# Performance work log

Measured on AMD Instinct MI355X. Metric: run time of the kernel, lower is better.

Reference implementation:

```python
import jax, jax.numpy as jnp
import numpy as np

B, C, H, W = 32, 256, 64, 64
MH = 8
E = 524288
TEMPERATURE = 0.1
LN_EPS = 1e-5


def setup_inputs() -> dict:
    key = jax.random.key(0)
    ks = jax.random.split(key, 6)
    n_nodes = B * H * W
    scale = 1.0 / np.sqrt(C).astype(np.float32)
    img = jax.random.normal(ks[0], (B, C, H, W), jnp.float32)
    all_edge = jax.random.randint(ks[1], (2, E), 0, n_nodes, dtype=jnp.int64)
    Wp = jax.random.normal(ks[2], (C, C), jnp.float32) * scale
    bp = jnp.zeros((C,), jnp.float32)
    Wg = jax.random.normal(ks[3], (C, C), jnp.float32) * scale
    bg = jnp.zeros((C,), jnp.float32)
    ln_gamma = jnp.ones((C,), jnp.float32)
    ln_beta = jnp.zeros((C,), jnp.float32)
    diff_query = jax.random.normal(ks[4], (1, 1, C), jnp.float32) * scale  # xavier-ish
    return {"img": img, "all_edge": all_edge, "Wp": Wp, "bp": bp,
            "Wg": Wg, "bg": bg, "ln_gamma": ln_gamma, "ln_beta": ln_beta,
            "diff_query": diff_query, "mask_head": MH}


def _gcn_conv(x, row, col, Wg, bg, num_nodes):
    # PyG GCNConv with add_self_loops=True, symmetric normalization.
    loop = jnp.arange(num_nodes, dtype=row.dtype)
    row = jnp.concatenate([row, loop])
    col = jnp.concatenate([col, loop])
    deg = jnp.zeros((num_nodes,), x.dtype).at[col].add(1.0)
    dinv = jnp.where(deg > 0, jax.lax.rsqrt(deg), 0.0)
    norm = dinv[row] * dinv[col]                      # [E+N]
    xl = x @ Wg                                       # [N, C]
    msg = xl[row] * norm[:, None]                     # gather + scale
    agg = jax.ops.segment_sum(msg, col, num_segments=num_nodes)
    return agg + bg


def reference(img, all_edge, Wp, bp, Wg, bg, ln_gamma, ln_beta, diff_query, mask_head):
    b, c, h, w = img.shape
    node_num = h * w
    num_nodes = b * node_num
    hd = c // mask_head
    # [B,C,H,W] -> [B, N, C]
    x = jnp.transpose(img, (0, 2, 3, 1)).reshape(b, node_num, c)
    x = x @ Wp + bp
    x = x.reshape(num_nodes, c)
    g = _gcn_conv(x, all_edge[0], all_edge[1], Wg, bg, num_nodes)
    g = jax.nn.gelu(g, approximate=False)             # nn.GELU (exact)
    g = g + x
    mu = jnp.mean(g, axis=-1, keepdims=True)
    var = jnp.mean(jnp.square(g - mu), axis=-1, keepdims=True)
    img_graph = (g - mu) * jax.lax.rsqrt(var + LN_EPS) * ln_gamma + ln_beta
    # multi-head adjacency: query [B*MH, 1, hd], keys [B*MH, N, hd]
    q = jnp.broadcast_to(diff_query, (b, 1, c)).reshape(b * mask_head, 1, hd)
    k = img_graph.reshape(b, node_num, mask_head, hd)
    k = jnp.transpose(k, (0, 2, 1, 3)).reshape(b * mask_head, node_num, hd)
    adj = jnp.einsum('bod,bnd->bon', q, k) / TEMPERATURE
    adj = jax.nn.softmax(adj, axis=-1)
    return img_graph, adj
```

## Files before the change

kernel.cpp:

```cpp
#include <hip/hip_runtime.h>

typedef unsigned short u16;
typedef __attribute__((ext_vector_type(8))) short short8;
typedef __attribute__((ext_vector_type(4))) float f32x4;
typedef __attribute__((ext_vector_type(16))) float f32x16;

#define AS1C(p) ((const __attribute__((address_space(1))) void*)(p))
#define AS3(p)  ((__attribute__((address_space(3))) void*)(p))

constexpr int CC    = 256;
constexpr int HWSZ  = 4096;
constexpr int NNODE = 131072;
constexpr int EEDG  = 524288;
constexpr int CAP   = 32;

__device__ __forceinline__ float bf2f(u16 h){ unsigned u = ((unsigned)h)<<16; float f; __builtin_memcpy(&f,&u,4); return f; }
__device__ __forceinline__ u16 f2bf(float f){ unsigned u; __builtin_memcpy(&u,&f,4); return (u16)((u + 0x7FFFu + ((u>>16)&1u))>>16); }
__device__ __forceinline__ float gelu_exact(float v){ return 0.5f*v*(1.0f + erff(v*0.7071067811865476f)); }

__device__ __forceinline__ void unpack8(uint4 q, float f[8]){
  unsigned w0=q.x,w1=q.y,w2=q.z,w3=q.w;
  unsigned l0=w0<<16, h0=w0&0xffff0000u, l1=w1<<16, h1=w1&0xffff0000u;
  unsigned l2=w2<<16, h2=w2&0xffff0000u, l3=w3<<16, h3=w3&0xffff0000u;
  __builtin_memcpy(&f[0],&l0,4); __builtin_memcpy(&f[1],&h0,4);
  __builtin_memcpy(&f[2],&l1,4); __builtin_memcpy(&f[3],&h1,4);
  __builtin_memcpy(&f[4],&l2,4); __builtin_memcpy(&f[5],&h2,4);
  __builtin_memcpy(&f[6],&l3,4); __builtin_memcpy(&f[7],&h3,4);
}

__global__ __launch_bounds__(256) void transpose_split(const float* __restrict__ src,
                                                       u16* __restrict__ dhi, u16* __restrict__ dlo,
                                                       int R, int Ccols, size_t sb_in, size_t sb_out)
{
  __shared__ float t[64][65];
  const float* s = src + blockIdx.z*sb_in + (size_t)(blockIdx.y*64)*Ccols + blockIdx.x*64;
  size_t obase   = blockIdx.z*sb_out + (size_t)(blockIdx.x*64)*R + blockIdx.y*64;
  int tid = threadIdx.x;
  for (int i=0;i<4;++i){
    int idx = i*256 + tid;
    int r = idx>>4, q = idx&15;
    float4 v = *(const float4*)(s + (size_t)r*Ccols + q*4);
    t[r][q*4+0]=v.x; t[r][q*4+1]=v.y; t[r][q*4+2]=v.z; t[r][q*4+3]=v.w;
  }
  __syncthreads();
  for (int i=0;i<2;++i){
    int idx = i*256 + tid;
    int rr = idx>>3, ch = idx&7;
    u16 hi[8], lo[8];
    for (int j=0;j<8;++j){
      float f = t[ch*8+j][rr];
      u16 h = f2bf(f); hi[j] = h;
      lo[j] = f2bf(f - bf2f(h));
    }
    *(uint4*)(dhi + obase + (size_t)rr*R + ch*8) = *(uint4*)hi;
    if (dlo) *(uint4*)(dlo + obase + (size_t)rr*R + ch*8) = *(uint4*)lo;
  }
}

__global__ __launch_bounds__(256,2) void gemm_img(const float* __restrict__ img,
                                                  const u16* __restrict__ Bt,
                                                  const float* __restrict__ bias,
                                                  u16* __restrict__ C)
{
  __shared__ float Afp[2][32*128];
  __shared__ u16   Bs[2][128*32];
  const int tid = threadIdx.x, wid = tid>>6, lane = tid&63;
  const int row0 = blockIdx.x*128, col0 = blockIdx.y*128;
  const int bb = row0 >> 12, hw0 = row0 & 4095;
  const float* abase = img + (size_t)bb*CC*HWSZ + hw0;
  const int wm = wid>>1, wn = wid&1;
  const int l31 = lane&31, lh = lane>>5;

  f32x16 acc[2][2];
  #pragma unroll
  for (int i=0;i<2;++i)
    #pragma unroll
    for (int j=0;j<2;++j)
      #pragma unroll
      for (int e=0;e<16;++e) acc[i][j][e]=0.f;

#define STAGE_IMG(buf, kt)                                                             \
  {                                                                                    \
    _Pragma("unroll")                                                                  \
    for (int it=0; it<4; ++it){                                                        \
      int qb = (it*4+wid)*64;                                                          \
      int q  = qb + lane;                                                              \
      int c  = q>>5, qq = q&31;                                                        \
      __builtin_amdgcn_global_load_lds(AS1C(abase + (size_t)((kt)+c)*HWSZ + qq*4),     \
                                       AS3(&Afp[buf][qb*4]), 16, 0, 0);                \
    }                                                                                  \
    _Pragma("unroll")                                                                  \
    for (int it=0; it<2; ++it){                                                        \
      int qb = (it*4+wid)*64;                                                          \
      int q  = qb + lane;                                                              \
      int m  = q>>2, sc = q&3;                                                         \
      int gs = sc ^ ((m>>1)&3);                                                        \
      __builtin_amdgcn_global_load_lds(AS1C(Bt + (size_t)(col0+m)*256 + (kt) + gs*8),  \
                                       AS3(&Bs[buf][qb*8]), 16, 0, 0);                 \
    }                                                                                  \
  }

  STAGE_IMG(0, 0)
  asm volatile("s_waitcnt vmcnt(0)" ::: "memory");
  __syncthreads();

  for (int t=0; t<8; ++t) {
    int cur = t&1;
    if (t<7) STAGE_IMG(cur^1, (t+1)*32)

    short8 ah[2][2], al[2][2], bfr[2][2];
    #pragma unroll
    for (int fm=0; fm<2; ++fm)
      #pragma unroll
      for (int kh=0; kh<2; ++kh) {
        int r  = wm*64 + fm*32 + l31;
        int cb = kh*16 + lh*8;
        #pragma unroll
        for (int j=0; j<8; ++j) {
          float f = Afp[cur][(cb+j)*128 + r];
          unsigned u; __builtin_memcpy(&u,&f,4);
          ah[fm][kh][j] = (short)(u>>16);
          unsigned uh = u & 0xffff0000u;
          float fh; __builtin_memcpy(&fh,&uh,4);
          float fl = f - fh;
          unsigned ul; __builtin_memcpy(&ul,&fl,4);
          al[fm][kh][j] = (short)(ul>>16);
        }
      }
    #pragma unroll
    for (int fn=0; fn<2; ++fn)
      #pragma unroll
      for (int kh=0; kh<2; ++kh) {
        int col = wn*64 + fn*32 + l31;
        int sb  = (kh*2 + lh) ^ ((col>>1)&3);
        bfr[fn][kh] = *(const short8*)&Bs[cur][col*32 + sb*8];
      }
    #pragma unroll
    for (int kh=0; kh<2; ++kh)
      #pragma unroll
      for (int fm=0; fm<2; ++fm)
        #pragma unroll
        for (int fn=0; fn<2; ++fn) {
          acc[fm][fn] = __builtin_amdgcn_mfma_f32_32x32x16_bf16(ah[fm][kh], bfr[fn][kh], acc[fm][fn], 0, 0, 0);
          acc[fm][fn] = __builtin_amdgcn_mfma_f32_32x32x16_bf16(al[fm][kh], bfr[fn][kh], acc[fm][fn], 0, 0, 0);
        }
    asm volatile("s_waitcnt vmcnt(0)" ::: "memory");
    __syncthreads();
  }
#undef STAGE_IMG

  #pragma unroll
  for (int fn=0; fn<2; ++fn) {
    int col = col0 + wn*64 + fn*32 + l31;
    float bv = bias ? bias[col] : 0.f;
    #pragma unroll
    for (int fm=0; fm<2; ++fm) {
      int rbase = row0 + wm*64 + fm*32 + 4*lh;
      #pragma unroll
      for (int reg=0; reg<16; ++reg) {
        int row = rbase + (reg&3) + 8*(reg>>2);
        C[(size_t)row*256 + col] = f2bf(acc[fm][fn][reg] + bv);
      }
    }
  }
}

__global__ __launch_bounds__(256,2) void gemm1p(const u16* __restrict__ A,
                                                const u16* __restrict__ Bt,
                                                u16* __restrict__ C)
{
  __shared__ u16 As[2][128*32];
  __shared__ u16 Bs[2][128*32];
  const int tid = threadIdx.x, wid = tid>>6, lane = tid&63;
  const int row0 = blockIdx.x*128, col0 = blockIdx.y*128;
  const int wm = wid>>1, wn = wid&1;
  const int l31 = lane&31, lh = lane>>5;

  f32x16 acc[2][2];
  #pragma unroll
  for (int i=0;i<2;++i)
    #pragma unroll
    for (int j=0;j<2;++j)
      #pragma unroll
      for (int e=0;e<16;++e) acc[i][j][e]=0.f;

#define STAGE_AB(buf, kt)                                                              \
  {                                                                                    \
    _Pragma("unroll")                                                                  \
    for (int it=0; it<2; ++it){                                                        \
      int qb = (it*4+wid)*64;                                                          \
      int q  = qb + lane;                                                              \
      int m  = q>>2, sc = q&3;                                                         \
      int gs = sc ^ ((m>>1)&3);                                                        \
      __builtin_amdgcn_global_load_lds(AS1C(A  + (size_t)(row0+m)*256 + (kt) + gs*8),  \
                                       AS3(&As[buf][qb*8]), 16, 0, 0);                 \
      __builtin_amdgcn_global_load_lds(AS1C(Bt + (size_t)(col0+m)*256 + (kt) + gs*8),  \
                                       AS3(&Bs[buf][qb*8]), 16, 0, 0);                 \
    }                                                                                  \
  }

  STAGE_AB(0, 0)
  asm volatile("s_waitcnt vmcnt(0)" ::: "memory");
  __syncthreads();

  for (int t=0; t<8; ++t) {
    int cur = t&1;
    if (t<7) STAGE_AB(cur^1, (t+1)*32)

    short8 af[2][2], bfr[2][2];
    #pragma unroll
    for (int fm=0; fm<2; ++fm)
      #pragma unroll
      for (int kh=0; kh<2; ++kh) {
        int row = wm*64 + fm*32 + l31;
        int sa  = (kh*2 + lh) ^ ((row>>1)&3);
        af[fm][kh] = *(const short8*)&As[cur][row*32 + sa*8];
      }
    #pragma unroll
    for (int fn=0; fn<2; ++fn)
      #pragma unroll
      for (int kh=0; kh<2; ++kh) {
        int col = wn*64 + fn*32 + l31;
        int sb  = (kh*2 + lh) ^ ((col>>1)&3);
        bfr[fn][kh] = *(const short8*)&Bs[cur][col*32 + sb*8];
      }
    #pragma unroll
    for (int kh=0; kh<2; ++kh)
      #pragma unroll
      for (int fm=0; fm<2; ++fm)
        #pragma unroll
        for (int fn=0; fn<2; ++fn)
          acc[fm][fn] = __builtin_amdgcn_mfma_f32_32x32x16_bf16(af[fm][kh], bfr[fn][kh], acc[fm][fn], 0, 0, 0);
    asm volatile("s_waitcnt vmcnt(0)" ::: "memory");
    __syncthreads();
  }
#undef STAGE_AB

  #pragma unroll
  for (int fn=0; fn<2; ++fn) {
    int col = col0 + wn*64 + fn*32 + l31;
    #pragma unroll
    for (int fm=0; fm<2; ++fm) {
      int rbase = row0 + wm*64 + fm*32 + 4*lh;
      #pragma unroll
      for (int reg=0; reg<16; ++reg) {
        int row = rbase + (reg&3) + 8*(reg>>2);
        C[(size_t)row*256 + col] = f2bf(acc[fm][fn][reg]);
      }
    }
  }
}

__global__ void fill_all(const int* __restrict__ row, const int* __restrict__ col,
                         int* __restrict__ cur, int* __restrict__ bucket){
  int e = blockIdx.x*256 + threadIdx.x;
  if (e >= EEDG) return;
  int c = col[e];
  int s = atomicAdd(&cur[c], 1);
  if (s < CAP) bucket[(size_t)c*CAP + s] = row[e];
}
__global__ void calc_dinv(const int* __restrict__ cnt, float* __restrict__ dinv){
  int n = blockIdx.x*256 + threadIdx.x;
  if (n < NNODE) dinv[n] = rsqrtf((float)cnt[n] + 1.0f);
}

__global__ __launch_bounds__(256) void fused_agg(
    const u16* __restrict__ xl, const u16* __restrict__ xhi,
    const int* __restrict__ cnt, const float* __restrict__ dinv, const int* __restrict__ bucket,
    const float* __restrict__ bgv, const float* __restrict__ gam, const float* __restrict__ bet,
    const float* __restrict__ qv, float* __restrict__ outg, float* __restrict__ logits)
{
  const int wid = threadIdx.x>>6, lane = threadIdx.x&63;
  const int half = lane>>5, sl = lane&31;
  const int n = blockIdx.x*8 + wid*2 + half;
  const int c0 = sl*8;
  const float dn = dinv[n];
  int lim = cnt[n]; if (lim > CAP) lim = CAP;

  int rl = bucket[(size_t)n*CAP + sl];
  if (sl >= lim) rl = n;
  float wl = (sl < lim) ? dinv[rl]*dn : 0.0f;

  float xv[8];
  uint4 qh = *(const uint4*)(xhi + (size_t)n*256 + c0);

  float a[8];
  {
    uint4 q = *(const uint4*)(xl + (size_t)n*256 + c0);
    unpack8(q, a);
    float wself = dn*dn;
    #pragma unroll
    for (int j=0;j<8;++j) a[j] *= wself;
  }

  int limR = (lim + 3) & ~3;
  for (int s=0; s<limR; s+=4) {
    int b0 = half*32 + s;
    int  r0 = __shfl(rl, b0),   r1 = __shfl(rl, b0+1);
    int  r2 = __shfl(rl, b0+2), r3 = __shfl(rl, b0+3);
    float w0 = __shfl(wl, b0),   w1 = __shfl(wl, b0+1);
    float w2 = __shfl(wl, b0+2), w3 = __shfl(wl, b0+3);
    uint4 q0 = *(const uint4*)(xl + (size_t)r0*256 + c0);
    uint4 q1 = *(const uint4*)(xl + (size_t)r1*256 + c0);
    uint4 q2 = *(const uint4*)(xl + (size_t)r2*256 + c0);
    uint4 q3 = *(const uint4*)(xl + (size_t)r3*256 + c0);
    float f0[8], f1[8], f2[8], f3[8];
    unpack8(q0, f0); unpack8(q1, f1); unpack8(q2, f2); unpack8(q3, f3);
    #pragma unroll
    for (int j=0;j<8;++j) a[j] += f0[j]*w0 + f1[j]*w1 + f2[j]*w2 + f3[j]*w3;
  }

  unpack8(qh, xv);

  float4 b0v = *(const float4*)(bgv + c0), b1v = *(const float4*)(bgv + c0 + 4);
  float bgs[8] = {b0v.x,b0v.y,b0v.z,b0v.w,b1v.x,b1v.y,b1v.z,b1v.w};
  float g[8];
  float s1 = 0.f, s2 = 0.f;
  #pragma unroll
  for (int j=0;j<8;++j){
    g[j] = gelu_exact(a[j] + bgs[j]) + xv[j];
    s1 += g[j]; s2 += g[j]*g[j];
  }
  #pragma unroll
  for (int off=16; off; off>>=1){ s1 += __shfl_xor(s1, off); s2 += __shfl_xor(s2, off); }
  float mu  = s1*(1.0f/256.0f);
  float var = s2*(1.0f/256.0f) - mu*mu;
  float inv = rsqrtf(var + 1e-5f);

  float4 g0 = *(const float4*)(gam + c0), g1 = *(const float4*)(gam + c0 + 4);
  float4 e0 = *(const float4*)(bet + c0), e1 = *(const float4*)(bet + c0 + 4);
  float gms[8] = {g0.x,g0.y,g0.z,g0.w,g1.x,g1.y,g1.z,g1.w};
  float bts[8] = {e0.x,e0.y,e0.z,e0.w,e1.x,e1.y,e1.z,e1.w};
  float y[8];
  #pragma unroll
  for (int j=0;j<8;++j) y[j] = (g[j]-mu)*inv*gms[j] + bts[j];

  f32x4 o0 = {y[0],y[1],y[2],y[3]}, o1 = {y[4],y[5],y[6],y[7]};
  __builtin_nontemporal_store(o0, (f32x4*)(outg + (size_t)n*256 + c0));
  __builtin_nontemporal_store(o1, (f32x4*)(outg + (size_t)n*256 + c0 + 4));

  float4 q0 = *(const float4*)(qv + c0), q1 = *(const float4*)(qv + c0 + 4);
  float qs[8] = {q0.x,q0.y,q0.z,q0.w,q1.x,q1.y,q1.z,q1.w};
  float dq = 0.f;
  #pragma unroll
  for (int j=0;j<8;++j) dq += y[j]*qs[j];
  dq += __shfl_xor(dq,1); dq += __shfl_xor(dq,2);
  if ((sl&3)==0){
    int b = n>>12, p = n&4095, h = sl>>2;
    logits[(size_t)(b*8+h)*4096 + p] = dq*10.0f;
  }
}

__global__ __launch_bounds__(256) void softmax_rows(const float* __restrict__ logits, float* __restrict__ outa){
  int r = blockIdx.x;
  const float* p = logits + (size_t)r*4096;
  int tid = threadIdx.x;
  int wid = tid>>6, lane = tid&63;
  __shared__ float redm[4];
  __shared__ float reds[4];
  float v[16];
  float mx = -1e30f;
  for (int i=0;i<16;++i){ v[i] = p[tid + i*256]; mx = fmaxf(mx, v[i]); }
  for (int off=32; off; off>>=1) mx = fmaxf(mx, __shfl_xor(mx, off));
  if (lane==0) redm[wid]=mx;
  __syncthreads();
  mx = fmaxf(fmaxf(redm[0],redm[1]), fmaxf(redm[2],redm[3]));
  float sum = 0.f;
  for (int i=0;i<16;++i){ v[i] = expf(v[i]-mx); sum += v[i]; }
  for (int off=32; off; off>>=1) sum += __shfl_xor(sum, off);
  if (lane==0) reds[wid]=sum;
  __syncthreads();
  sum = reds[0]+reds[1]+reds[2]+reds[3];
  float rinv = 1.0f/sum;
  for (int i=0;i<16;++i) outa[(size_t)r*4096 + tid + i*256] = v[i]*rinv;
}

extern "C" void kernel_launch(void* const* d_in, const int* in_sizes, int n_in,
                              void* d_out, int out_size, void* d_ws, size_t ws_size,
                              hipStream_t stream)
{
  const float* img  = (const float*)d_in[0];
  const int* edges  = (const int*)d_in[1];
  const float* Wp   = (const float*)d_in[2];
  const float* bp   = (const float*)d_in[3];
  const float* Wg   = (const float*)d_in[4];
  const float* bg   = (const float*)d_in[5];
  const float* lng  = (const float*)d_in[6];
  const float* lnb  = (const float*)d_in[7];
  const float* dq   = (const float*)d_in[8];
  char* ws = (char*)d_ws;

  constexpr size_t REG  = (size_t)NNODE*CC*2;
  constexpr size_t WTS  = 2u*131072;
  constexpr size_t GBLK = 524288u*2 + (size_t)NNODE*CAP*4 + (size_t)256*4096*4;
  if (ws_size < 2*REG + WTS + GBLK) return;

  u16* x_hi = (u16*)(ws + 0);
  u16* xl   = (u16*)(ws + REG);
  char* wts  = ws + 2*REG;
  char* gblk = wts + WTS;

  u16* WpT_hi = (u16*)(wts);
  u16* WgT_hi = (u16*)(wts + 131072);
  int*   cur    = (int*)(gblk);
  float* dinv   = (float*)(gblk + 524288);
  int*   bucket = (int*)(gblk + 1048576);
  float* logits = (float*)(gblk + 1048576 + (size_t)NNODE*CAP*4);

  transpose_split<<<dim3(4,4,1), 256, 0, stream>>>(Wp, WpT_hi, nullptr, 256, 256, 0, 0);
  transpose_split<<<dim3(4,4,1), 256, 0, stream>>>(Wg, WgT_hi, nullptr, 256, 256, 0, 0);

  hipMemsetAsync(cur, 0, 524288, stream);
  fill_all <<<2048, 256, 0, stream>>>(edges, edges+EEDG, cur, bucket);
  calc_dinv<<<512,  256, 0, stream>>>(cur, dinv);

  gemm_img<<<dim3(1024,2), 256, 0, stream>>>(img, WpT_hi, bp, x_hi);
  gemm1p<<<dim3(1024,2), 256, 0, stream>>>(x_hi, WgT_hi, xl);

  float* outg = (float*)d_out;
  float* outa = (float*)d_out + (size_t)NNODE*CC;
  fused_agg<<<NNODE/8, 256, 0, stream>>>(xl, x_hi, cur, dinv, bucket,
                                         bg, lng, lnb, dq, outg, logits);
  softmax_rows<<<256, 256, 0, stream>>>(logits, outa);
}
```

Measured before the change: 242.5 us.

## Retile GEMMs to 64x256 blocks covering full output width

Both projection GEMMs switch from 128x128 tiles on a 2D grid to 64-row by 256-column tiles on a 1D grid. Each block now reads its A rows (the image, or the projected features) once instead of twice, and each of the four waves owns a 64-column slice. This cuts duplicate A-side global traffic, especially the fp32 image reads with hi/lo splitting, at the cost of staging more B per block and larger LDS for B. The aggregation kernel also swaps its nontemporal output stores for plain float4 stores.

```diff
diff --git a/kernel.cpp b/kernel.cpp
--- a/kernel.cpp
+++ b/kernel.cpp
@@ -62,13 +62,12 @@
                                                   const float* __restrict__ bias,
                                                   u16* __restrict__ C)
 {
-  __shared__ float Afp[2][32*128];
-  __shared__ u16   Bs[2][128*32];
+  __shared__ float Afp[2][32*64];
+  __shared__ u16   Bs[2][256*32];
   const int tid = threadIdx.x, wid = tid>>6, lane = tid&63;
-  const int row0 = blockIdx.x*128, col0 = blockIdx.y*128;
+  const int row0 = blockIdx.x*64;
   const int bb = row0 >> 12, hw0 = row0 & 4095;
   const float* abase = img + (size_t)bb*CC*HWSZ + hw0;
-  const int wm = wid>>1, wn = wid&1;
   const int l31 = lane&31, lh = lane>>5;
 
   f32x16 acc[2][2];
@@ -81,21 +80,21 @@
 
 #define STAGE_IMG(buf, kt)                                                             \
   {                                                                                    \
+    _Pragma("unroll")                                                                  \
+    for (int it=0; it<2; ++it){                                                        \
+      int qb = (it*4+wid)*64;                                                          \
+      int q  = qb + lane;                                                              \
+      int c  = q>>4, mq = q&15;                                                        \
+      __builtin_amdgcn_global_load_lds(AS1C(abase + (size_t)((kt)+c)*HWSZ + mq*4),     \
+                                       AS3(&Afp[buf][qb*4]), 16, 0, 0);                \
+    }                                                                                  \
     _Pragma("unroll")                                                                  \
     for (int it=0; it<4; ++it){                                                        \
       int qb = (it*4+wid)*64;                                                          \
       int q  = qb + lane;                                                              \
-      int c  = q>>5, qq = q&31;                                                        \
-      __builtin_amdgcn_global_load_lds(AS1C(abase + (size_t)((kt)+c)*HWSZ + qq*4),     \
-                                       AS3(&Afp[buf][qb*4]), 16, 0, 0);                \
-    }                                                                                  \
-    _Pragma("unroll")                                                                  \
-    for (int it=0; it<2; ++it){                                                        \
-      int qb = (it*4+wid)*64;                                                          \
-      int q  = qb + lane;                                                              \
       int m  = q>>2, sc = q&3;                                                         \
       int gs = sc ^ ((m>>1)&3);                                                        \
-      __builtin_amdgcn_global_load_lds(AS1C(Bt + (size_t)(col0+m)*256 + (kt) + gs*8),  \
+      __builtin_amdgcn_global_load_lds(AS1C(Bt + (size_t)m*256 + (kt) + gs*8),         \
                                        AS3(&Bs[buf][qb*8]), 16, 0, 0);                 \
     }                                                                                  \
   }
@@ -113,11 +112,11 @@
     for (int fm=0; fm<2; ++fm)
       #pragma unroll
       for (int kh=0; kh<2; ++kh) {
-        int r  = wm*64 + fm*32 + l31;
+        int r  = fm*32 + l31;
         int cb = kh*16 + lh*8;
         #pragma unroll
         for (int j=0; j<8; ++j) {
-          float f = Afp[cur][(cb+j)*128 + r];
+          float f = Afp[cur][(cb+j)*64 + r];
           unsigned u; __builtin_memcpy(&u,&f,4);
           ah[fm][kh][j] = (short)(u>>16);
           unsigned uh = u & 0xffff0000u;
@@ -131,7 +130,7 @@
     for (int fn=0; fn<2; ++fn)
       #pragma unroll
       for (int kh=0; kh<2; ++kh) {
-        int col = wn*64 + fn*32 + l31;
+        int col = wid*64 + fn*32 + l31;
         int sb  = (kh*2 + lh) ^ ((col>>1)&3);
         bfr[fn][kh] = *(const short8*)&Bs[cur][col*32 + sb*8];
       }
@@ -151,11 +150,11 @@
 
   #pragma unroll
   for (int fn=0; fn<2; ++fn) {
-    int col = col0 + wn*64 + fn*32 + l31;
+    int col = wid*64 + fn*32 + l31;
     float bv = bias ? bias[col] : 0.f;
     #pragma unroll
     for (int fm=0; fm<2; ++fm) {
-      int rbase = row0 + wm*64 + fm*32 + 4*lh;
+      int rbase = row0 + fm*32 + 4*lh;
       #pragma unroll
       for (int reg=0; reg<16; ++reg) {
         int row = rbase + (reg&3) + 8*(reg>>2);
@@ -169,11 +168,10 @@
                                                 const u16* __restrict__ Bt,
                                                 u16* __restrict__ C)
 {
-  __shared__ u16 As[2][128*32];
-  __shared__ u16 Bs[2][128*32];
+  __shared__ u16 As[2][64*32];
+  __shared__ u16 Bs[2][256*32];
   const int tid = threadIdx.x, wid = tid>>6, lane = tid&63;
-  const int row0 = blockIdx.x*128, col0 = blockIdx.y*128;
-  const int wm = wid>>1, wn = wid&1;
+  const int row0 = blockIdx.x*64;
   const int l31 = lane&31, lh = lane>>5;
 
   f32x16 acc[2][2];
@@ -186,15 +184,21 @@
 
 #define STAGE_AB(buf, kt)                                                              \
   {                                                                                    \
+    {                                                                                  \
+      int qb = wid*64;                                                                 \
+      int q  = qb + lane;                                                              \
+      int m  = q>>2, sc = q&3;                                                         \
+      int gs = sc ^ ((m>>1)&3);                                                        \
+      __builtin_amdgcn_global_load_lds(AS1C(A + (size_t)(row0+m)*256 + (kt) + gs*8),   \
+                                       AS3(&As[buf][qb*8]), 16, 0, 0);                 \
+    }                                                                                  \
     _Pragma("unroll")                                                                  \
-    for (int it=0; it<2; ++it){                                                        \
+    for (int it=0; it<4; ++it){                                                        \
       int qb = (it*4+wid)*64;                                                          \
       int q  = qb + lane;                                                              \
       int m  = q>>2, sc = q&3;                                                         \
       int gs = sc ^ ((m>>1)&3);                                                        \
-      __builtin_amdgcn_global_load_lds(AS1C(A  + (size_t)(row0+m)*256 + (kt) + gs*8),  \
-                                       AS3(&As[buf][qb*8]), 16, 0, 0);                 \
-      __builtin_amdgcn_global_load_lds(AS1C(Bt + (size_t)(col0+m)*256 + (kt) + gs*8),  \
+      __builtin_amdgcn_global_load_lds(AS1C(Bt + (size_t)m*256 + (kt) + gs*8),         \
                                        AS3(&Bs[buf][qb*8]), 16, 0, 0);                 \
     }                                                                                  \
   }
@@ -212,7 +216,7 @@
     for (int fm=0; fm<2; ++fm)
       #pragma unroll
       for (int kh=0; kh<2; ++kh) {
-        int row = wm*64 + fm*32 + l31;
+        int row = fm*32 + l31;
         int sa  = (kh*2 + lh) ^ ((row>>1)&3);
         af[fm][kh] = *(const short8*)&As[cur][row*32 + sa*8];
       }
@@ -220,7 +224,7 @@
     for (int fn=0; fn<2; ++fn)
       #pragma unroll
       for (int kh=0; kh<2; ++kh) {
-        int col = wn*64 + fn*32 + l31;
+        int col = wid*64 + fn*32 + l31;
         int sb  = (kh*2 + lh) ^ ((col>>1)&3);
         bfr[fn][kh] = *(const short8*)&Bs[cur][col*32 + sb*8];
       }
@@ -238,10 +242,10 @@
 
   #pragma unroll
   for (int fn=0; fn<2; ++fn) {
-    int col = col0 + wn*64 + fn*32 + l31;
+    int col = wid*64 + fn*32 + l31;
     #pragma unroll
     for (int fm=0; fm<2; ++fm) {
-      int rbase = row0 + wm*64 + fm*32 + 4*lh;
+      int rbase = row0 + fm*32 + 4*lh;
       #pragma unroll
       for (int reg=0; reg<16; ++reg) {
         int row = rbase + (reg&3) + 8*(reg>>2);
@@ -281,7 +285,6 @@
   if (sl >= lim) rl = n;
   float wl = (sl < lim) ? dinv[rl]*dn : 0.0f;
 
-  float xv[8];
   uint4 qh = *(const uint4*)(xhi + (size_t)n*256 + c0);
 
   float a[8];
@@ -310,6 +313,7 @@
     for (int j=0;j<8;++j) a[j] += f0[j]*w0 + f1[j]*w1 + f2[j]*w2 + f3[j]*w3;
   }
 
+  float xv[8];
   unpack8(qh, xv);
 
   float4 b0v = *(const float4*)(bgv + c0), b1v = *(const float4*)(bgv + c0 + 4);
@@ -335,9 +339,9 @@
   #pragma unroll
   for (int j=0;j<8;++j) y[j] = (g[j]-mu)*inv*gms[j] + bts[j];
 
-  f32x4 o0 = {y[0],y[1],y[2],y[3]}, o1 = {y[4],y[5],y[6],y[7]};
-  __builtin_nontemporal_store(o0, (f32x4*)(outg + (size_t)n*256 + c0));
-  __builtin_nontemporal_store(o1, (f32x4*)(outg + (size_t)n*256 + c0 + 4));
+  float4 o0 = {y[0],y[1],y[2],y[3]}, o1 = {y[4],y[5],y[6],y[7]};
+  *reinterpret_cast<float4*>(outg + (size_t)n*256 + c0)     = o0;
+  *reinterpret_cast<float4*>(outg + (size_t)n*256 + c0 + 4) = o1;
 
   float4 q0 = *(const float4*)(qv + c0), q1 = *(const float4*)(qv + c0 + 4);
   float qs[8] = {q0.x,q0.y,q0.z,q0.w,q1.x,q1.y,q1.z,q1.w};
@@ -414,8 +418,8 @@
   fill_all <<<2048, 256, 0, stream>>>(edges, edges+EEDG, cur, bucket);
   calc_dinv<<<512,  256, 0, stream>>>(cur, dinv);
 
-  gemm_img<<<dim3(1024,2), 256, 0, stream>>>(img, WpT_hi, bp, x_hi);
-  gemm1p<<<dim3(1024,2), 256, 0, stream>>>(x_hi, WgT_hi, xl);
+  gemm_img<<<2048, 256, 0, stream>>>(img, WpT_hi, bp, x_hi);
+  gemm1p<<<2048, 256, 0, stream>>>(x_hi, WgT_hi, xl);
 
   float* outg = (float*)d_out;
   float* outa = (float*)d_out + (size_t)NNODE*CC;
```

Result: faster. 237.0 us (-2.3%).
